# Performance work log

Hardware: AMD Instinct MI355X
Metric: run time of the kernel (lower is better)

## Reference

```python
import jax, jax.numpy as jnp
import numpy as np

NEG_INF = -1e9  # large negative for masking (avoid NaN rows under -inf with fully masked rows)
LEAKY_SLOPE = 0.2

def setup_inputs() -> dict:
    key = jax.random.key(0)
    k1, k2, k3, k4, k5 = jax.random.split(key, 5)
    N, in_dim, out_dim = 8192, 512, 64
    x = jax.random.normal(k1, (N, in_dim), dtype=jnp.float32)
    adj = jax.random.randint(k2, (N, N), 0, 2, dtype=jnp.int32)
    W = jax.random.normal(k3, (out_dim, in_dim), dtype=jnp.float32) * (1.0 / np.sqrt(in_dim))
    a_src = jax.random.normal(k4, (out_dim,), dtype=jnp.float32)
    a_dst = jax.random.normal(k5, (out_dim,), dtype=jnp.float32)
    return {"x": x, "adj": adj, "W": W, "a_src": a_src, "a_dst": a_dst}

def reference(x, adj, W, a_src, a_dst):
    # Linear projection: Wh[n, d]
    Wh = x @ W.T
    # Additive GAT attention: e[i, j] = LeakyReLU(a_src . Wh_i + a_dst . Wh_j)
    s = Wh @ a_src  # [N]
    d = Wh @ a_dst  # [N]
    e = jax.nn.leaky_relu(s[:, None] + d[None, :], negative_slope=LEAKY_SLOPE)  # [N, N]
    e = jnp.where(adj > 0, e, NEG_INF)
    alpha = jax.nn.softmax(e, axis=1)  # [N, N]
    # Dropout on alpha is identity in eval/reference mode.
    h_prime = alpha @ Wh  # [N, out_dim]
    return h_prime
```

## Files before the change

kernel.cpp:

```cpp
#include <hip/hip_runtime.h>

#define GN 8192
#define IN_DIM 512
#define ODIM 64
#define SLOPE 0.2f
#define JSPLIT 16
#define JCH (GN / JSPLIT)
#define LSTRIDE 68

typedef __attribute__((ext_vector_type(4))) float  f32x4;
typedef __attribute__((ext_vector_type(4))) int    i32x4;
typedef __attribute__((ext_vector_type(8))) short  bf16x8;
typedef __attribute__((ext_vector_type(4))) unsigned short u16x4;

static __device__ __forceinline__ float bf2f(unsigned short u) {
    return __uint_as_float(((unsigned)u) << 16);
}
static __device__ __forceinline__ unsigned short f2bf(float f) {
    union { float f; unsigned u; } c; c.f = f;
    unsigned b = c.u;
    return (unsigned short)((b + 0x7fffu + ((b >> 16) & 1u)) >> 16);
}

static __device__ __forceinline__ bf16x8 load8(const void* p, size_t off, int f32) {
    if (f32) {
        f32x4 lo = *(const f32x4*)((const float*)p + off);
        f32x4 hi = *(const f32x4*)((const float*)p + off + 4);
        bf16x8 r;
        #pragma unroll
        for (int q = 0; q < 4; ++q) {
            r[q]     = (short)f2bf(lo[q]);
            r[4 + q] = (short)f2bf(hi[q]);
        }
        return r;
    }
    return *(const bf16x8*)((const ushort*)p + off);
}

extern "C" __global__ __launch_bounds__(256)
void gat_proj(const void* __restrict__ x_, const void* __restrict__ W_,
              const void* __restrict__ as_, const void* __restrict__ ad_,
              ushort* __restrict__ WhT, float* __restrict__ s_arr,
              float* __restrict__ d_arr, int* __restrict__ dmax_bits,
              int* __restrict__ dflag)
{
    const int wave = threadIdx.x >> 6;
    const int lane = threadIdx.x & 63;
    unsigned xw = ((const unsigned*)x_)[lane];
    unsigned ef = (xw >> 23) & 0xffu;
    unsigned long long vt = __ballot(ef > 60u && ef < 180u);
    const int f32 = (__popcll(vt) >= 32) ? 1 : 0;
    if (blockIdx.x == 0 && threadIdx.x == 0) *dflag = f32;

    const int quad = lane >> 4;
    const int lq   = lane & 15;
    const int i0   = blockIdx.x * 64 + wave * 16;

    f32x4 acc[4] = {{0,0,0,0},{0,0,0,0},{0,0,0,0},{0,0,0,0}};
    const size_t arow = (size_t)(i0 + lq) * IN_DIM;
    #pragma unroll 2
    for (int k0 = 0; k0 < IN_DIM; k0 += 32) {
        const int kk = k0 + quad * 8;
        bf16x8 a  = load8(x_, arow + kk, f32);
        bf16x8 b0 = load8(W_, (size_t)( 0 + lq) * IN_DIM + kk, f32);
        bf16x8 b1 = load8(W_, (size_t)(16 + lq) * IN_DIM + kk, f32);
        bf16x8 b2 = load8(W_, (size_t)(32 + lq) * IN_DIM + kk, f32);
        bf16x8 b3 = load8(W_, (size_t)(48 + lq) * IN_DIM + kk, f32);
        acc[0] = __builtin_amdgcn_mfma_f32_16x16x32_bf16(a, b0, acc[0], 0, 0, 0);
        acc[1] = __builtin_amdgcn_mfma_f32_16x16x32_bf16(a, b1, acc[1], 0, 0, 0);
        acc[2] = __builtin_amdgcn_mfma_f32_16x16x32_bf16(a, b2, acc[2], 0, 0, 0);
        acc[3] = __builtin_amdgcn_mfma_f32_16x16x32_bf16(a, b3, acc[3], 0, 0, 0);
    }
    float av_s[4], av_d[4];
    #pragma unroll
    for (int t = 0; t < 4; ++t) {
        const int n = t * 16 + lq;
        av_s[t] = f32 ? ((const float*)as_)[n] : bf2f(((const ushort*)as_)[n]);
        av_d[t] = f32 ? ((const float*)ad_)[n] : bf2f(((const ushort*)ad_)[n]);
    }
    #pragma unroll
    for (int t = 0; t < 4; ++t) {
        u16x4 pk;
        #pragma unroll
        for (int r = 0; r < 4; ++r) pk[r] = f2bf(acc[t][r]);
        *(u16x4*)(WhT + (size_t)(t * 16 + lq) * GN + i0 + quad * 4) = pk;
    }
    float ps[4], pd[4];
    #pragma unroll
    for (int r = 0; r < 4; ++r) {
        float s = 0.f, d = 0.f;
        #pragma unroll
        for (int t = 0; t < 4; ++t) {
            s = fmaf(acc[t][r], av_s[t], s);
            d = fmaf(acc[t][r], av_d[t], d);
        }
        #pragma unroll
        for (int off = 1; off < 16; off <<= 1) {
            s += __shfl_xor(s, off);
            d += __shfl_xor(d, off);
        }
        ps[r] = s; pd[r] = d;
    }
    if (lq == 0) {
        float dmx = -1e30f;
        #pragma unroll
        for (int r = 0; r < 4; ++r) {
            s_arr[i0 + quad * 4 + r] = ps[r];
            d_arr[i0 + quad * 4 + r] = pd[r];
            dmx = fmaxf(dmx, pd[r]);
        }
        if (dmx > 0.f) atomicMax(dmax_bits, __float_as_int(dmx));
    }
}

extern "C" __global__ __launch_bounds__(256)
void gat_attn(const int* __restrict__ adj, const ushort* __restrict__ WhT,
              const float* __restrict__ s_arr, const float* __restrict__ d_arr,
              const int* __restrict__ dmax_bits,
              float* __restrict__ accum, float* __restrict__ lsum)
{
    __shared__ unsigned char mb[64 * LSTRIDE];
    const int ib   = blockIdx.x & 127;
    const int js   = blockIdx.x >> 7;
    const int wave = threadIdx.x >> 6;
    const int lane = threadIdx.x & 63;
    const int quad = lane >> 4;
    const int lq   = lane & 15;
    const int i0   = ib * 64;
    const int jbase = js * JCH;

    #pragma unroll 4
    for (int s = 0; s < 16; ++s) {
        const int r = s * 4 + wave;
        const int* row = adj + (size_t)(i0 + r) * GN + jbase;
        i32x4 a0 = *(const i32x4*)(row + lane * 8);
        i32x4 a1 = *(const i32x4*)(row + lane * 8 + 4);
        unsigned byte = 0;
        #pragma unroll
        for (int q = 0; q < 4; ++q) {
            byte |= (a0[q] > 0 ? 1u : 0u) << q;
            byte |= (a1[q] > 0 ? 1u : 0u) << (4 + q);
        }
        mb[r * LSTRIDE + lane] = (unsigned char)byte;
    }
    __syncthreads();

    const int li = wave * 16 + lq;
    const int i  = i0 + li;
    const float dmax = __int_as_float(*dmax_bits);
    const float si = s_arr[i];
    const float tb = si + dmax;
    const float mi = fmaxf(tb, SLOPE * tb);
    f32x4 acc0 = {0,0,0,0}, acc1 = {0,0,0,0}, acc2 = {0,0,0,0}, acc3 = {0,0,0,0};
    f32x4 acc4 = {0,0,0,0};
    bf16x8 ones;
    #pragma unroll
    for (int q = 0; q < 8; ++q) ones[q] = (short)0x3F80;

    #pragma unroll 2
    for (int it = 0; it < JCH / 32; ++it) {
        const int j0 = jbase + it * 32 + quad * 8;
        unsigned bw = *(const unsigned*)(mb + li * LSTRIDE + it * 4);
        const unsigned m8 = (bw >> (quad * 8)) & 0xffu;
        f32x4 dv0 = *(const f32x4*)(d_arr + j0);
        f32x4 dv1 = *(const f32x4*)(d_arr + j0 + 4);
        bf16x8 b0 = *(const bf16x8*)(WhT + (size_t)( 0 + lq) * GN + j0);
        bf16x8 b1 = *(const bf16x8*)(WhT + (size_t)(16 + lq) * GN + j0);
        bf16x8 b2 = *(const bf16x8*)(WhT + (size_t)(32 + lq) * GN + j0);
        bf16x8 b3 = *(const bf16x8*)(WhT + (size_t)(48 + lq) * GN + j0);
        float w[8];
        #pragma unroll
        for (int q = 0; q < 4; ++q) {
            float e0 = si + dv0[q];
            e0 = fmaxf(e0, SLOPE * e0);
            float v0 = __expf(e0 - mi);
            w[q] = ((m8 >> q) & 1u) ? v0 : 0.f;
            float e1 = si + dv1[q];
            e1 = fmaxf(e1, SLOPE * e1);
            float v1 = __expf(e1 - mi);
            w[4 + q] = ((m8 >> (4 + q)) & 1u) ? v1 : 0.f;
        }
        bf16x8 af;
        #pragma unroll
        for (int q = 0; q < 8; ++q) af[q] = (short)f2bf(w[q]);
        acc0 = __builtin_amdgcn_mfma_f32_16x16x32_bf16(af, b0, acc0, 0, 0, 0);
        acc1 = __builtin_amdgcn_mfma_f32_16x16x32_bf16(af, b1, acc1, 0, 0, 0);
        acc2 = __builtin_amdgcn_mfma_f32_16x16x32_bf16(af, b2, acc2, 0, 0, 0);
        acc3 = __builtin_amdgcn_mfma_f32_16x16x32_bf16(af, b3, acc3, 0, 0, 0);
        acc4 = __builtin_amdgcn_mfma_f32_16x16x32_bf16(af, ones, acc4, 0, 0, 0);
    }
    const int orow = i0 + wave * 16 + quad * 4;
    if (lq == 0) {
        #pragma unroll
        for (int r = 0; r < 4; ++r) atomicAdd(&lsum[orow + r], acc4[r]);
    }
    #pragma unroll
    for (int r = 0; r < 4; ++r) {
        atomicAdd(&accum[(size_t)(orow + r) * ODIM +  0 + lq], acc0[r]);
        atomicAdd(&accum[(size_t)(orow + r) * ODIM + 16 + lq], acc1[r]);
        atomicAdd(&accum[(size_t)(orow + r) * ODIM + 32 + lq], acc2[r]);
        atomicAdd(&accum[(size_t)(orow + r) * ODIM + 48 + lq], acc3[r]);
    }
}

extern "C" __global__ __launch_bounds__(256)
void gat_final(const float* __restrict__ accum, const float* __restrict__ lsum,
               const int* __restrict__ flag, void* __restrict__ out)
{
    const int idx = blockIdx.x * 256 + threadIdx.x;
    const float v = accum[idx] / lsum[idx >> 6];
    if (*flag) ((float*)out)[idx] = v;
    else       ((ushort*)out)[idx] = f2bf(v);
}

extern "C" void kernel_launch(void* const* d_in, const int* in_sizes, int n_in,
                              void* d_out, int out_size, void* d_ws, size_t ws_size,
                              hipStream_t stream)
{
    const void* x     = d_in[0];
    const int*  adj   = (const int*)d_in[1];
    const void* W     = d_in[2];
    const void* a_src = d_in[3];
    const void* a_dst = d_in[4];

    char* ws = (char*)d_ws;
    size_t off = 0;
    float* accum = (float*)(ws + off);  off += (size_t)GN * ODIM * 4;
    float* lsum  = (float*)(ws + off);  off += (size_t)GN * 4;
    int* dmax_bits = (int*)(ws + off);  off += 128;
    size_t zero_bytes = off;
    int* dflag = (int*)(ws + off);      off += 128;
    float* s_arr = (float*)(ws + off);  off += (size_t)GN * 4;
    float* d_arr = (float*)(ws + off);  off += (size_t)GN * 4;
    ushort* WhT  = (ushort*)(ws + off); off += (size_t)ODIM * GN * 2;

    hipMemsetAsync(ws, 0, zero_bytes, stream);
    gat_proj<<<GN / 64, 256, 0, stream>>>(x, W, a_src, a_dst,
                                          WhT, s_arr, d_arr, dmax_bits, dflag);
    gat_attn<<<128 * JSPLIT, 256, 0, stream>>>(adj, WhT, s_arr, d_arr,
                                               dmax_bits, accum, lsum);
    gat_final<<<GN * ODIM / 256, 256, 0, stream>>>(accum, lsum, dflag, d_out);
}
```

Measured before the change: 463.6 us.

## Make attention blocks persistent over four column tiles with double-buffered adjacency prefetch

Cuts the attention grid to 512 blocks, each handling four column chunks with stride 4*JCH, so fewer atomic flushes happen per output row. The adjacency bitmask for the next tile is loaded into registers and packed into a second shared buffer while the current tile computes. WhT and d values are also register-prefetched one iteration ahead. This aims to hide the dominant adj HBM read latency behind MFMA work, at the cost of more registers and fewer blocks in flight.

```diff
diff --git a/kernel.cpp b/kernel.cpp
--- a/kernel.cpp
+++ b/kernel.cpp
@@ -7,6 +7,7 @@
 #define JSPLIT 16
 #define JCH (GN / JSPLIT)
 #define LSTRIDE 68
+#define NTILE 4
 
 typedef __attribute__((ext_vector_type(4))) float  f32x4;
 typedef __attribute__((ext_vector_type(4))) int    i32x4;
@@ -119,76 +120,118 @@
               const int* __restrict__ dmax_bits,
               float* __restrict__ accum, float* __restrict__ lsum)
 {
-    __shared__ unsigned char mb[64 * LSTRIDE];
-    const int ib   = blockIdx.x & 127;
-    const int js   = blockIdx.x >> 7;
+    __shared__ unsigned char mb[2][64 * LSTRIDE];
+    const int b    = blockIdx.x;
+    const int ib   = b & 127;
+    const int js0  = b >> 7;
     const int wave = threadIdx.x >> 6;
     const int lane = threadIdx.x & 63;
     const int quad = lane >> 4;
     const int lq   = lane & 15;
     const int i0   = ib * 64;
-    const int jbase = js * JCH;
-
-    #pragma unroll 4
-    for (int s = 0; s < 16; ++s) {
-        const int r = s * 4 + wave;
-        const int* row = adj + (size_t)(i0 + r) * GN + jbase;
-        i32x4 a0 = *(const i32x4*)(row + lane * 8);
-        i32x4 a1 = *(const i32x4*)(row + lane * 8 + 4);
-        unsigned byte = 0;
-        #pragma unroll
-        for (int q = 0; q < 4; ++q) {
-            byte |= (a0[q] > 0 ? 1u : 0u) << q;
-            byte |= (a1[q] > 0 ? 1u : 0u) << (4 + q);
-        }
-        mb[r * LSTRIDE + lane] = (unsigned char)byte;
-    }
-    __syncthreads();
-
-    const int li = wave * 16 + lq;
-    const int i  = i0 + li;
+    const int li   = wave * 16 + lq;
+    const int i    = i0 + li;
     const float dmax = __int_as_float(*dmax_bits);
     const float si = s_arr[i];
-    const float tb = si + dmax;
-    const float mi = fmaxf(tb, SLOPE * tb);
+    const float tbv = si + dmax;
+    const float mi = fmaxf(tbv, SLOPE * tbv);
+
+    const size_t adjbase = (size_t)i0 * GN + lane * 8;
+
+    i32x4 ra[3], rb[3];
+    auto pack = [&](const i32x4& va, const i32x4& vb, int c, int bufsel) {
+        unsigned byte = 0;
+        #pragma unroll
+        for (int q = 0; q < 4; ++q) {
+            byte |= (va[q] > 0 ? 1u : 0u) << q;
+            byte |= (vb[q] > 0 ? 1u : 0u) << (4 + q);
+        }
+        mb[bufsel][(c * 4 + wave) * LSTRIDE + lane] = (unsigned char)byte;
+    };
+
     f32x4 acc0 = {0,0,0,0}, acc1 = {0,0,0,0}, acc2 = {0,0,0,0}, acc3 = {0,0,0,0};
     f32x4 acc4 = {0,0,0,0};
     bf16x8 ones;
     #pragma unroll
     for (int q = 0; q < 8; ++q) ones[q] = (short)0x3F80;
 
-    #pragma unroll 2
-    for (int it = 0; it < JCH / 32; ++it) {
-        const int j0 = jbase + it * 32 + quad * 8;
-        unsigned bw = *(const unsigned*)(mb + li * LSTRIDE + it * 4);
-        const unsigned m8 = (bw >> (quad * 8)) & 0xffu;
-        f32x4 dv0 = *(const f32x4*)(d_arr + j0);
-        f32x4 dv1 = *(const f32x4*)(d_arr + j0 + 4);
-        bf16x8 b0 = *(const bf16x8*)(WhT + (size_t)( 0 + lq) * GN + j0);
-        bf16x8 b1 = *(const bf16x8*)(WhT + (size_t)(16 + lq) * GN + j0);
-        bf16x8 b2 = *(const bf16x8*)(WhT + (size_t)(32 + lq) * GN + j0);
-        bf16x8 b3 = *(const bf16x8*)(WhT + (size_t)(48 + lq) * GN + j0);
-        float w[8];
-        #pragma unroll
-        for (int q = 0; q < 4; ++q) {
-            float e0 = si + dv0[q];
-            e0 = fmaxf(e0, SLOPE * e0);
-            float v0 = __expf(e0 - mi);
-            w[q] = ((m8 >> q) & 1u) ? v0 : 0.f;
-            float e1 = si + dv1[q];
-            e1 = fmaxf(e1, SLOPE * e1);
-            float v1 = __expf(e1 - mi);
-            w[4 + q] = ((m8 >> (4 + q)) & 1u) ? v1 : 0.f;
-        }
-        bf16x8 af;
-        #pragma unroll
-        for (int q = 0; q < 8; ++q) af[q] = (short)f2bf(w[q]);
-        acc0 = __builtin_amdgcn_mfma_f32_16x16x32_bf16(af, b0, acc0, 0, 0, 0);
-        acc1 = __builtin_amdgcn_mfma_f32_16x16x32_bf16(af, b1, acc1, 0, 0, 0);
-        acc2 = __builtin_amdgcn_mfma_f32_16x16x32_bf16(af, b2, acc2, 0, 0, 0);
-        acc3 = __builtin_amdgcn_mfma_f32_16x16x32_bf16(af, b3, acc3, 0, 0, 0);
-        acc4 = __builtin_amdgcn_mfma_f32_16x16x32_bf16(af, ones, acc4, 0, 0, 0);
-    }
+    {
+        const int jb = js0 * JCH;
+        #pragma unroll
+        for (int c = 0; c < 16; ++c) {
+            const int* rp = adj + adjbase + (size_t)(c * 4 + wave) * GN + jb;
+            ra[c % 3] = ((const i32x4*)rp)[0];
+            rb[c % 3] = ((const i32x4*)rp)[1];
+            if (c >= 2) pack(ra[(c - 2) % 3], rb[(c - 2) % 3], c - 2, 0);
+        }
+        pack(ra[14 % 3], rb[14 % 3], 14, 0);
+        pack(ra[15 % 3], rb[15 % 3], 15, 0);
+    }
+    __syncthreads();
+
+    int jpre = js0 * JCH + quad * 8;
+    f32x4 dv0 = *(const f32x4*)(d_arr + jpre);
+    f32x4 dv1 = *(const f32x4*)(d_arr + jpre + 4);
+    bf16x8 b0 = *(const bf16x8*)(WhT + (size_t)( 0 + lq) * GN + jpre);
+    bf16x8 b1 = *(const bf16x8*)(WhT + (size_t)(16 + lq) * GN + jpre);
+    bf16x8 b2 = *(const bf16x8*)(WhT + (size_t)(32 + lq) * GN + jpre);
+    bf16x8 b3 = *(const bf16x8*)(WhT + (size_t)(48 + lq) * GN + jpre);
+
+    #pragma unroll 1
+    for (int t = 0; t < NTILE; ++t) {
+        const int jb   = (js0 + 4 * t) * JCH;
+        const int jbn  = jb + 4 * JCH;
+        const bool more = (t < NTILE - 1);
+        const int buf  = t & 1, nbuf = buf ^ 1;
+
+        #pragma unroll
+        for (int it = 0; it < 16; ++it) {
+            const int jn = (it < 15) ? (jb + (it + 1) * 32 + quad * 8)
+                                     : (more ? (jbn + quad * 8) : (jb + quad * 8));
+            f32x4 ndv0 = *(const f32x4*)(d_arr + jn);
+            f32x4 ndv1 = *(const f32x4*)(d_arr + jn + 4);
+            bf16x8 nb0 = *(const bf16x8*)(WhT + (size_t)( 0 + lq) * GN + jn);
+            bf16x8 nb1 = *(const bf16x8*)(WhT + (size_t)(16 + lq) * GN + jn);
+            bf16x8 nb2 = *(const bf16x8*)(WhT + (size_t)(32 + lq) * GN + jn);
+            bf16x8 nb3 = *(const bf16x8*)(WhT + (size_t)(48 + lq) * GN + jn);
+            if (more) {
+                const int* rp = adj + adjbase + (size_t)(it * 4 + wave) * GN + jbn;
+                ra[it % 3] = ((const i32x4*)rp)[0];
+                rb[it % 3] = ((const i32x4*)rp)[1];
+            }
+            if (more && it >= 2)
+                pack(ra[(it - 2) % 3], rb[(it - 2) % 3], it - 2, nbuf);
+            unsigned bw = *(const unsigned*)(&mb[buf][li * LSTRIDE + it * 4]);
+            const unsigned m8 = (bw >> (quad * 8)) & 0xffu;
+            float w[8];
+            #pragma unroll
+            for (int q = 0; q < 4; ++q) {
+                float e0 = si + dv0[q];
+                e0 = fmaxf(e0, SLOPE * e0);
+                float v0 = __expf(e0 - mi);
+                w[q] = ((m8 >> q) & 1u) ? v0 : 0.f;
+                float e1 = si + dv1[q];
+                e1 = fmaxf(e1, SLOPE * e1);
+                float v1 = __expf(e1 - mi);
+                w[4 + q] = ((m8 >> (4 + q)) & 1u) ? v1 : 0.f;
+            }
+            bf16x8 af;
+            #pragma unroll
+            for (int q = 0; q < 8; ++q) af[q] = (short)f2bf(w[q]);
+            acc0 = __builtin_amdgcn_mfma_f32_16x16x32_bf16(af, b0, acc0, 0, 0, 0);
+            acc1 = __builtin_amdgcn_mfma_f32_16x16x32_bf16(af, b1, acc1, 0, 0, 0);
+            acc2 = __builtin_amdgcn_mfma_f32_16x16x32_bf16(af, b2, acc2, 0, 0, 0);
+            acc3 = __builtin_amdgcn_mfma_f32_16x16x32_bf16(af, b3, acc3, 0, 0, 0);
+            acc4 = __builtin_amdgcn_mfma_f32_16x16x32_bf16(af, ones, acc4, 0, 0, 0);
+            dv0 = ndv0; dv1 = ndv1; b0 = nb0; b1 = nb1; b2 = nb2; b3 = nb3;
+        }
+        if (more) {
+            pack(ra[14 % 3], rb[14 % 3], 14, nbuf);
+            pack(ra[15 % 3], rb[15 % 3], 15, nbuf);
+        }
+        __syncthreads();
+    }
+
     const int orow = i0 + wave * 16 + quad * 4;
     if (lq == 0) {
         #pragma unroll
@@ -237,7 +280,7 @@
     hipMemsetAsync(ws, 0, zero_bytes, stream);
     gat_proj<<<GN / 64, 256, 0, stream>>>(x, W, a_src, a_dst,
                                           WhT, s_arr, d_arr, dmax_bits, dflag);
-    gat_attn<<<128 * JSPLIT, 256, 0, stream>>>(adj, WhT, s_arr, d_arr,
-                                               dmax_bits, accum, lsum);
+    gat_attn<<<512, 256, 0, stream>>>(adj, WhT, s_arr, d_arr,
+                                      dmax_bits, accum, lsum);
     gat_final<<<GN * ODIM / 256, 256, 0, stream>>>(accum, lsum, dflag, d_out);
 }
```

Measured after the change: 441.0 us. 1.05x faster.

## Stream adjacency tiles into LDS with double-buffered async loads and packed Wh layout

Applied to the files above, without the earlier changes.

The attention kernel now copies the int32 adjacency into double-buffered LDS tiles with global_load_lds, using an XOR swizzle, and prefetches the next tile while computing on the current one. Before, it compressed the mask into bitmasks up front. Wh is stored in a packed 8-column-group layout so each MFMA B-fragment load is contiguous. The grid shrinks from 2048 to 512 blocks, each covering 2048 columns over 16 tiles, which cuts atomic traffic but leaves fewer blocks and uses 64 KB of LDS per block.

```diff
diff --git a/kernel.cpp b/kernel.cpp
--- a/kernel.cpp
+++ b/kernel.cpp
@@ -4,14 +4,16 @@
 #define IN_DIM 512
 #define ODIM 64
 #define SLOPE 0.2f
-#define JSPLIT 16
-#define JCH (GN / JSPLIT)
-#define LSTRIDE 68
+#define TCOLS 128
+#define NT 16
 
 typedef __attribute__((ext_vector_type(4))) float  f32x4;
 typedef __attribute__((ext_vector_type(4))) int    i32x4;
 typedef __attribute__((ext_vector_type(8))) short  bf16x8;
 typedef __attribute__((ext_vector_type(4))) unsigned short u16x4;
+
+typedef __attribute__((address_space(1))) const unsigned gu32;
+typedef __attribute__((address_space(3))) unsigned       lu32;
 
 static __device__ __forceinline__ float bf2f(unsigned short u) {
     return __uint_as_float(((unsigned)u) << 16);
@@ -40,7 +42,7 @@
 extern "C" __global__ __launch_bounds__(256)
 void gat_proj(const void* __restrict__ x_, const void* __restrict__ W_,
               const void* __restrict__ as_, const void* __restrict__ ad_,
-              ushort* __restrict__ WhT, float* __restrict__ s_arr,
+              ushort* __restrict__ WhTp, float* __restrict__ s_arr,
               float* __restrict__ d_arr, int* __restrict__ dmax_bits,
               int* __restrict__ dflag)
 {
@@ -83,7 +85,9 @@
         u16x4 pk;
         #pragma unroll
         for (int r = 0; r < 4; ++r) pk[r] = f2bf(acc[t][r]);
-        *(u16x4*)(WhT + (size_t)(t * 16 + lq) * GN + i0 + quad * 4) = pk;
+        const size_t hw = ((size_t)((i0 >> 3) + (quad >> 1)) * 64 + t * 16 + lq) * 8
+                          + (quad & 1) * 4;
+        *(u16x4*)(WhTp + hw) = pk;
     }
     float ps[4], pd[4];
     #pragma unroll
@@ -113,82 +117,112 @@
     }
 }
 
-extern "C" __global__ __launch_bounds__(256)
-void gat_attn(const int* __restrict__ adj, const ushort* __restrict__ WhT,
+extern "C" __global__ __launch_bounds__(256, 2)
+void gat_attn(const int* __restrict__ adj, const ushort* __restrict__ WhTp,
               const float* __restrict__ s_arr, const float* __restrict__ d_arr,
               const int* __restrict__ dmax_bits,
               float* __restrict__ accum, float* __restrict__ lsum)
 {
-    __shared__ unsigned char mb[64 * LSTRIDE];
-    const int ib   = blockIdx.x & 127;
-    const int js   = blockIdx.x >> 7;
+    __shared__ int adjbuf[2][64 * TCOLS];
+    const int b    = blockIdx.x;
+    const int ib   = b & 127;
+    const int jq   = b >> 7;
     const int wave = threadIdx.x >> 6;
     const int lane = threadIdx.x & 63;
     const int quad = lane >> 4;
     const int lq   = lane & 15;
     const int i0   = ib * 64;
-    const int jbase = js * JCH;
-
-    #pragma unroll 4
-    for (int s = 0; s < 16; ++s) {
-        const int r = s * 4 + wave;
-        const int* row = adj + (size_t)(i0 + r) * GN + jbase;
-        i32x4 a0 = *(const i32x4*)(row + lane * 8);
-        i32x4 a1 = *(const i32x4*)(row + lane * 8 + 4);
-        unsigned byte = 0;
-        #pragma unroll
-        for (int q = 0; q < 4; ++q) {
-            byte |= (a0[q] > 0 ? 1u : 0u) << q;
-            byte |= (a1[q] > 0 ? 1u : 0u) << (4 + q);
-        }
-        mb[r * LSTRIDE + lane] = (unsigned char)byte;
-    }
-    __syncthreads();
-
-    const int li = wave * 16 + lq;
-    const int i  = i0 + li;
+    const int li   = wave * 16 + lq;
+    const int i    = i0 + li;
     const float dmax = __int_as_float(*dmax_bits);
     const float si = s_arr[i];
-    const float tb = si + dmax;
-    const float mi = fmaxf(tb, SLOPE * tb);
+    const float tbv = si + dmax;
+    const float mi = fmaxf(tbv, SLOPE * tbv);
+
+    const int rloc = 2 * (wave * 8) + (lane >> 5);
+    (void)rloc;
+    const int s32  = lane & 31;
+
     f32x4 acc0 = {0,0,0,0}, acc1 = {0,0,0,0}, acc2 = {0,0,0,0}, acc3 = {0,0,0,0};
     f32x4 acc4 = {0,0,0,0};
     bf16x8 ones;
     #pragma unroll
     for (int q = 0; q < 8; ++q) ones[q] = (short)0x3F80;
 
-    #pragma unroll 2
-    for (int it = 0; it < JCH / 32; ++it) {
-        const int j0 = jbase + it * 32 + quad * 8;
-        unsigned bw = *(const unsigned*)(mb + li * LSTRIDE + it * 4);
-        const unsigned m8 = (bw >> (quad * 8)) & 0xffu;
-        f32x4 dv0 = *(const f32x4*)(d_arr + j0);
-        f32x4 dv1 = *(const f32x4*)(d_arr + j0 + 4);
-        bf16x8 b0 = *(const bf16x8*)(WhT + (size_t)( 0 + lq) * GN + j0);
-        bf16x8 b1 = *(const bf16x8*)(WhT + (size_t)(16 + lq) * GN + j0);
-        bf16x8 b2 = *(const bf16x8*)(WhT + (size_t)(32 + lq) * GN + j0);
-        bf16x8 b3 = *(const bf16x8*)(WhT + (size_t)(48 + lq) * GN + j0);
-        float w[8];
-        #pragma unroll
-        for (int q = 0; q < 4; ++q) {
-            float e0 = si + dv0[q];
-            e0 = fmaxf(e0, SLOPE * e0);
-            float v0 = __expf(e0 - mi);
-            w[q] = ((m8 >> q) & 1u) ? v0 : 0.f;
-            float e1 = si + dv1[q];
-            e1 = fmaxf(e1, SLOPE * e1);
-            float v1 = __expf(e1 - mi);
-            w[4 + q] = ((m8 >> (4 + q)) & 1u) ? v1 : 0.f;
-        }
-        bf16x8 af;
-        #pragma unroll
-        for (int q = 0; q < 8; ++q) af[q] = (short)f2bf(w[q]);
-        acc0 = __builtin_amdgcn_mfma_f32_16x16x32_bf16(af, b0, acc0, 0, 0, 0);
-        acc1 = __builtin_amdgcn_mfma_f32_16x16x32_bf16(af, b1, acc1, 0, 0, 0);
-        acc2 = __builtin_amdgcn_mfma_f32_16x16x32_bf16(af, b2, acc2, 0, 0, 0);
-        acc3 = __builtin_amdgcn_mfma_f32_16x16x32_bf16(af, b3, acc3, 0, 0, 0);
-        acc4 = __builtin_amdgcn_mfma_f32_16x16x32_bf16(af, ones, acc4, 0, 0, 0);
-    }
+    const int jb0 = jq * (NT * TCOLS);
+
+    #pragma unroll
+    for (int c = 0; c < 8; ++c) {
+        const int R = wave * 8 + c;
+        const int r = 2 * R + (lane >> 5);
+        const int g = s32 ^ (r & 31);
+        const int* gp = adj + (size_t)(i0 + r) * GN + jb0 + g * 4;
+        void* lp = (char*)&adjbuf[0][0] + R * 1024;
+        __builtin_amdgcn_global_load_lds((gu32*)(const void*)gp, (lu32*)lp, 16, 0, 0);
+    }
+    __syncthreads();
+
+    #pragma unroll 1
+    for (int t = 0; t < NT; ++t) {
+        const int jb = jb0 + t * TCOLS;
+        f32x4 dva[4][2];
+        bf16x8 bfa[4][4];
+        #pragma unroll
+        for (int it = 0; it < 4; ++it) {
+            const int j0 = jb + it * 32 + quad * 8;
+            dva[it][0] = *(const f32x4*)(d_arr + j0);
+            dva[it][1] = *(const f32x4*)(d_arr + j0 + 4);
+            const ushort* nb = WhTp + ((size_t)(jb >> 3) + it * 4 + quad) * 512;
+            bfa[it][0] = *(const bf16x8*)(nb + ( 0 + lq) * 8);
+            bfa[it][1] = *(const bf16x8*)(nb + (16 + lq) * 8);
+            bfa[it][2] = *(const bf16x8*)(nb + (32 + lq) * 8);
+            bfa[it][3] = *(const bf16x8*)(nb + (48 + lq) * 8);
+        }
+        __builtin_amdgcn_sched_barrier(0);
+        if (t < NT - 1) {
+            const int jbn = jb + TCOLS;
+            #pragma unroll
+            for (int c = 0; c < 8; ++c) {
+                const int R = wave * 8 + c;
+                const int r = 2 * R + (lane >> 5);
+                const int g = s32 ^ (r & 31);
+                const int* gp = adj + (size_t)(i0 + r) * GN + jbn + g * 4;
+                void* lp = (char*)&adjbuf[(t + 1) & 1][0] + R * 1024;
+                __builtin_amdgcn_global_load_lds((gu32*)(const void*)gp, (lu32*)lp, 16, 0, 0);
+            }
+        }
+        __builtin_amdgcn_sched_barrier(0);
+        const char* buf = (const char*)&adjbuf[t & 1][0];
+        #pragma unroll
+        for (int it = 0; it < 4; ++it) {
+            const int u0 = it * 8 + 2 * quad;
+            const int sw = li & 31;
+            i32x4 av0 = *(const i32x4*)(buf + li * 512 + ((u0     ^ sw) * 16));
+            i32x4 av1 = *(const i32x4*)(buf + li * 512 + (((u0+1) ^ sw) * 16));
+            float w[8];
+            #pragma unroll
+            for (int q = 0; q < 4; ++q) {
+                float e0 = si + dva[it][0][q];
+                e0 = fmaxf(e0, SLOPE * e0);
+                float v0 = __expf(e0 - mi);
+                w[q] = (av0[q] > 0) ? v0 : 0.f;
+                float e1 = si + dva[it][1][q];
+                e1 = fmaxf(e1, SLOPE * e1);
+                float v1 = __expf(e1 - mi);
+                w[4 + q] = (av1[q] > 0) ? v1 : 0.f;
+            }
+            bf16x8 af;
+            #pragma unroll
+            for (int q = 0; q < 8; ++q) af[q] = (short)f2bf(w[q]);
+            acc0 = __builtin_amdgcn_mfma_f32_16x16x32_bf16(af, bfa[it][0], acc0, 0, 0, 0);
+            acc1 = __builtin_amdgcn_mfma_f32_16x16x32_bf16(af, bfa[it][1], acc1, 0, 0, 0);
+            acc2 = __builtin_amdgcn_mfma_f32_16x16x32_bf16(af, bfa[it][2], acc2, 0, 0, 0);
+            acc3 = __builtin_amdgcn_mfma_f32_16x16x32_bf16(af, bfa[it][3], acc3, 0, 0, 0);
+            acc4 = __builtin_amdgcn_mfma_f32_16x16x32_bf16(af, ones, acc4, 0, 0, 0);
+        }
+        __syncthreads();
+    }
+
     const int orow = i0 + wave * 16 + quad * 4;
     if (lq == 0) {
         #pragma unroll
@@ -232,12 +266,12 @@
     int* dflag = (int*)(ws + off);      off += 128;
     float* s_arr = (float*)(ws + off);  off += (size_t)GN * 4;
     float* d_arr = (float*)(ws + off);  off += (size_t)GN * 4;
-    ushort* WhT  = (ushort*)(ws + off); off += (size_t)ODIM * GN * 2;
+    ushort* WhTp = (ushort*)(ws + off); off += (size_t)ODIM * GN * 2;
 
     hipMemsetAsync(ws, 0, zero_bytes, stream);
     gat_proj<<<GN / 64, 256, 0, stream>>>(x, W, a_src, a_dst,
-                                          WhT, s_arr, d_arr, dmax_bits, dflag);
-    gat_attn<<<128 * JSPLIT, 256, 0, stream>>>(adj, WhT, s_arr, d_arr,
-                                               dmax_bits, accum, lsum);
+                                          WhTp, s_arr, d_arr, dmax_bits, dflag);
+    gat_attn<<<512, 256, 0, stream>>>(adj, WhTp, s_arr, d_arr,
+                                      dmax_bits, accum, lsum);
     gat_final<<<GN * ODIM / 256, 256, 0, stream>>>(accum, lsum, dflag, d_out);
 }
```

Measured after the change: 454.5 us. Within noise of the previous version (-2.0%).
